# Kernel tuning notes

Hardware: AMD Instinct MI355X
Metric: run time of the kernel (lower is better)

The kernel has to match this reference:

```python
import jax, jax.numpy as jnp
import numpy as np

DIM = 768
HID = 3072  # 4 * DIM
EPS = 1e-5


def layer_norm(x, w, b):
    mu = jnp.mean(x, axis=-1, keepdims=True)
    var = jnp.var(x, axis=-1, keepdims=True)
    return (x - mu) * jax.lax.rsqrt(var + EPS) * w + b


def setup_inputs() -> dict:
    key = jax.random.key(0)
    ks = jax.random.split(key, 8)
    C, H = DIM, HID
    s = lambda fan_in: 1.0 / np.sqrt(fan_in)
    return {
        "x": jax.random.normal(ks[0], (32, 577, C), dtype=jnp.float32),
        "norm1_w": jnp.ones((C,), jnp.float32),
        "norm1_b": jnp.zeros((C,), jnp.float32),
        "qkv_w": jax.random.uniform(ks[1], (3 * C, C), jnp.float32, -s(C), s(C)),
        "proj_w": jax.random.uniform(ks[2], (C, C), jnp.float32, -s(C), s(C)),
        "proj_b": jax.random.uniform(ks[3], (C,), jnp.float32, -s(C), s(C)),
        "norm2_w": jnp.ones((C,), jnp.float32),
        "norm2_b": jnp.zeros((C,), jnp.float32),
        "fc1_w": jax.random.uniform(ks[4], (H, C), jnp.float32, -s(C), s(C)),
        "fc1_b": jax.random.uniform(ks[5], (H,), jnp.float32, -s(C), s(C)),
        "fc2_w": jax.random.uniform(ks[6], (C, H), jnp.float32, -s(H), s(H)),
        "fc2_b": jax.random.uniform(ks[7], (C,), jnp.float32, -s(H), s(H)),
    }


def reference(x, norm1_w, norm1_b, qkv_w, proj_w, proj_b,
              norm2_w, norm2_b, fc1_w, fc1_b, fc2_w, fc2_b):
    B, N, C = x.shape
    attn_size = int((N - 1) ** 0.5)
    scale = C ** -0.5

    # --- Attention on norm1(x) (single head) ---
    h = layer_norm(x, norm1_w, norm1_b)
    qkv = (h @ qkv_w.T).reshape(B, N, 3, C)           # [B,N,3,C]
    q, k, v = qkv[:, :, 0], qkv[:, :, 1], qkv[:, :, 2]
    attn = jax.nn.softmax(jnp.einsum('bnc,bmc->bnm', q, k) * scale, axis=-1)
    y = jnp.einsum('bnm,bmc->bnc', attn, v)           # [B,N,C]
    # Faithful to torch: .transpose(1,2).reshape(B,N,C) scrambles layout
    y = jnp.transpose(y, (0, 2, 1)).reshape(B, N, C)
    a = y @ proj_w.T + proj_b
    token_attn = attn[:, 0, 1:].reshape(B, 1, attn_size, attn_size)

    # Faithful to torch Block: input residual is discarded, attention out doubled
    x = a + a

    # --- MLP (exact GELU, as nn.GELU default) ---
    m = layer_norm(x, norm2_w, norm2_b)
    m = jax.nn.gelu(m @ fc1_w.T + fc1_b, approximate=False)
    m = m @ fc2_w.T + fc2_b
    x = x + m
    return (x, token_attn)
```

## Files before the change

### kernel.cpp

```cpp
#include <hip/hip_runtime.h>
#include <hip/hip_bf16.h>

#define Bz   32
#define Nn_  577
#define Np   640
#define Cc   768
#define Hh   3072
#define Mrows (Bz * Nn_)
#define OUT_X (Mrows * Cc)
#define SCALE 0.03608439182435161f

typedef unsigned short ushort_t;
typedef short short8 __attribute__((ext_vector_type(8)));
typedef float f32x4 __attribute__((ext_vector_type(4)));

__device__ __forceinline__ ushort_t f2b(float f) {
    __hip_bfloat16 h = __float2bfloat16(f);
    return *reinterpret_cast<ushort_t*>(&h);
}

__device__ __forceinline__ void gl16(const ushort_t* g, ushort_t* l) {
    __builtin_amdgcn_global_load_lds(
        (const __attribute__((address_space(1))) void*)g,
        (__attribute__((address_space(3))) void*)l, 16, 0, 0);
}

__device__ __forceinline__ float bsum(float v, float* sm) {
    #pragma unroll
    for (int o = 32; o > 0; o >>= 1) v += __shfl_down(v, o, 64);
    int lane = threadIdx.x & 63, wid = threadIdx.x >> 6;
    if (lane == 0) sm[wid] = v;
    __syncthreads();
    float r = sm[0] + sm[1] + sm[2] + sm[3];
    __syncthreads();
    return r;
}
__device__ __forceinline__ float bmax(float v, float* sm) {
    #pragma unroll
    for (int o = 32; o > 0; o >>= 1) v = fmaxf(v, __shfl_down(v, o, 64));
    int lane = threadIdx.x & 63, wid = threadIdx.x >> 6;
    if (lane == 0) sm[wid] = v;
    __syncthreads();
    float r = fmaxf(fmaxf(sm[0], sm[1]), fmaxf(sm[2], sm[3]));
    __syncthreads();
    return r;
}

__global__ void cvt_kernel(const float* __restrict__ in, ushort_t* __restrict__ out, int n) {
    int i = blockIdx.x * 256 + threadIdx.x;
    if (i < n) out[i] = f2b(in[i]);
}

__global__ void ln_bf16(const float* __restrict__ x, const float* __restrict__ w,
                        const float* __restrict__ b, ushort_t* __restrict__ out) {
    __shared__ float sm[8];
    long long row = blockIdx.x;
    const float* xr = x + row * Cc;
    float v[3]; float s = 0.f;
    #pragma unroll
    for (int i = 0; i < 3; ++i) { v[i] = xr[threadIdx.x + i * 256]; s += v[i]; }
    float mu = bsum(s, sm) * (1.f / (float)Cc);
    float sq = 0.f;
    #pragma unroll
    for (int i = 0; i < 3; ++i) { float d = v[i] - mu; sq += d * d; }
    float var = bsum(sq, sm + 4) * (1.f / (float)Cc);
    float inv = rsqrtf(var + 1e-5f);
    ushort_t* orow = out + row * Cc;
    #pragma unroll
    for (int i = 0; i < 3; ++i) {
        int c = threadIdx.x + i * 256;
        orow[c] = f2b((v[i] - mu) * inv * w[c] + b[c]);
    }
}

__global__ void softmax_bf16(const float* __restrict__ Sf, ushort_t* __restrict__ Sb,
                             float* __restrict__ tok) {
    __shared__ float sm[8];
    long long row = blockIdx.x;
    int b_l = (int)(row / Nn_), r = (int)(row - (long long)b_l * Nn_);
    const float* src = Sf + row * Np;
    ushort_t* dst = Sb + row * Np;
    float v[3]; float mx = -1e30f;
    #pragma unroll
    for (int i = 0; i < 3; ++i) {
        int c = threadIdx.x + i * 256;
        v[i] = (c < Nn_) ? src[c] : -1e30f;
        mx = fmaxf(mx, v[i]);
    }
    mx = bmax(mx, sm);
    float s = 0.f;
    #pragma unroll
    for (int i = 0; i < 3; ++i) {
        int c = threadIdx.x + i * 256;
        v[i] = (c < Nn_) ? expf(v[i] - mx) : 0.f;
        s += v[i];
    }
    s = bsum(s, sm + 4);
    float inv = 1.f / s;
    #pragma unroll
    for (int i = 0; i < 3; ++i) {
        int c = threadIdx.x + i * 256;
        float p = v[i] * inv;
        if (c < Np) dst[c] = (c < Nn_) ? f2b(p) : (ushort_t)0;
        if (r == 0 && c >= 1 && c < Nn_) tok[(long long)b_l * 576 + (c - 1)] = p;
    }
}

#define EPS_STORE 0
#define EPS_X2    1
#define EPS_GELU  2
#define EPS_ACC   3
#define EPS_QKV   4

template<int EPI, typename OutT>
__global__ __launch_bounds__(256)
void mm_bf16(const ushort_t* __restrict__ A, long long sAb, int lda, int M,
             const ushort_t* __restrict__ B, long long sBb, int ldb, int Nv,
             const float* __restrict__ bias,
             OutT* __restrict__ O, long long sOb, int ldo,
             int K, float alpha,
             ushort_t* __restrict__ qQ, ushort_t* __restrict__ qK, ushort_t* __restrict__ qV)
{
    __shared__ __align__(16) ushort_t As[128 * 32];
    __shared__ __align__(16) ushort_t Bs[128 * 32];
    const int z = blockIdx.z;
    A += (long long)z * sAb; B += (long long)z * sBb;
    if (O) O += (long long)z * sOb;
    const int n0 = blockIdx.x * 128;
    const int m0 = blockIdx.y * 128;
    const int tid = threadIdx.x;
    const int lane = tid & 63;
    const int wv = tid >> 6;
    const int wr = (wv >> 1) << 6;
    const int wc = (wv & 1) << 6;
    const int fr = lane & 15;
    const int koff = (lane >> 4) * 8;

    const int e0 = tid * 8, e1 = 2048 + tid * 8;
    const int ra0 = e0 >> 5, ca0 = e0 & 31;
    const int ra1 = e1 >> 5, ca1 = e1 & 31;
    const ushort_t* Ag0 = A + (long long)min(m0 + ra0, M - 1) * lda + ca0;
    const ushort_t* Ag1 = A + (long long)min(m0 + ra1, M - 1) * lda + ca1;
    const ushort_t* Bg0 = B + (long long)min(n0 + ra0, Nv - 1) * ldb + ca0;
    const ushort_t* Bg1 = B + (long long)min(n0 + ra1, Nv - 1) * ldb + ca1;

    f32x4 acc[4][4] = {};

    for (int k0 = 0; k0 < K; k0 += 32) {
        gl16(Ag0 + k0, &As[e0]);
        gl16(Ag1 + k0, &As[e1]);
        gl16(Bg0 + k0, &Bs[e0]);
        gl16(Bg1 + k0, &Bs[e1]);
        __syncthreads();
        short8 af[4], bfr[4];
        #pragma unroll
        for (int i = 0; i < 4; ++i)
            af[i] = *(const short8*)&As[(wr + i * 16 + fr) * 32 + koff];
        #pragma unroll
        for (int j = 0; j < 4; ++j)
            bfr[j] = *(const short8*)&Bs[(wc + j * 16 + fr) * 32 + koff];
        #pragma unroll
        for (int i = 0; i < 4; ++i)
            #pragma unroll
            for (int j = 0; j < 4; ++j)
                acc[i][j] = __builtin_amdgcn_mfma_f32_16x16x32_bf16(af[i], bfr[j], acc[i][j], 0, 0, 0);
        __syncthreads();
    }

    #pragma unroll
    for (int i = 0; i < 4; ++i) {
        int mb = m0 + wr + i * 16 + (lane >> 4) * 4;
        #pragma unroll
        for (int j = 0; j < 4; ++j) {
            int n = n0 + wc + j * 16 + fr;
            if (n >= Nv) continue;
            f32x4 v4 = acc[i][j];
            #pragma unroll
            for (int r = 0; r < 4; ++r) {
                int m = mb + r;
                if (m >= M) continue;
                float v = v4[r] * alpha;
                if constexpr (EPI == EPS_QKV) {
                    int b_l = m / Nn_, rr = m - b_l * Nn_;
                    if (n < Cc)            qQ[(long long)m * Cc + n] = f2b(v);
                    else if (n < 2 * Cc)   qK[(long long)m * Cc + (n - Cc)] = f2b(v);
                    else                   qV[((long long)b_l * Cc + (n - 2 * Cc)) * Np + rr] = f2b(v);
                } else {
                    if (bias) v += bias[n];
                    if constexpr (EPI == EPS_X2) v *= 2.f;
                    if constexpr (EPI == EPS_GELU) v = 0.5f * v * (1.f + erff(v * 0.70710678118654752f));
                    long long oi = (long long)m * ldo + n;
                    if constexpr (EPI == EPS_ACC) {
                        O[oi] += v;
                    } else {
                        if constexpr (sizeof(OutT) == 2) O[oi] = (OutT)f2b(v);
                        else                             O[oi] = (OutT)v;
                    }
                }
            }
        }
    }
}

extern "C" void kernel_launch(void* const* d_in, const int* in_sizes, int n_in,
                              void* d_out, int out_size, void* d_ws, size_t ws_size,
                              hipStream_t stream) {
    const float* x      = (const float*)d_in[0];
    const float* n1w    = (const float*)d_in[1];
    const float* n1b    = (const float*)d_in[2];
    const float* qkv_w  = (const float*)d_in[3];
    const float* proj_w = (const float*)d_in[4];
    const float* proj_b = (const float*)d_in[5];
    const float* n2w    = (const float*)d_in[6];
    const float* n2b    = (const float*)d_in[7];
    const float* fc1w   = (const float*)d_in[8];
    const float* fc1b   = (const float*)d_in[9];
    const float* fc2w   = (const float*)d_in[10];
    const float* fc2b   = (const float*)d_in[11];
    float* out = (float*)d_out;
    float* x2  = out;
    float* tok = out + OUT_X;

    char* ws = (char*)d_ws;
    const long long nWq = (long long)3 * Cc * Cc;
    const long long nWp = (long long)Cc * Cc;
    const long long nW1 = (long long)Hh * Cc;
    const long long nW2 = (long long)Cc * Hh;
    ushort_t* wq = (ushort_t*)ws;
    ushort_t* wp = wq + nWq;
    ushort_t* w1 = wp + nWp;
    ushort_t* w2 = w1 + nW1;
    const long long WBYTES = 2 * (nWq + nWp + nW1 + nW2);
    char* dyn = ws + WBYTES;
    long long avail = (long long)ws_size - WBYTES;

    const long long perG = 3LL * Nn_ * Cc * 2 + (long long)Cc * Np * 2
                         + (long long)Nn_ * Np * 4 + (long long)Nn_ * Np * 2;
    int G = 1;
    { const int o[5] = {16, 8, 4, 2, 1};
      for (int i = 0; i < 5; ++i) if ((long long)o[i] * perG <= avail) { G = o[i]; break; } }
    int CH = Nn_;
    { const int o[5] = {16, 8, 4, 2, 1};
      for (int i = 0; i < 5; ++i) if ((long long)o[i] * Nn_ * (Cc + Hh) * 2 <= avail) { CH = o[i] * Nn_; break; } }

    ushort_t* hbf = (ushort_t*)dyn;
    ushort_t* Q   = hbf + (long long)G * Nn_ * Cc;
    ushort_t* Kb  = Q   + (long long)G * Nn_ * Cc;
    ushort_t* Vt  = Kb  + (long long)G * Nn_ * Cc;
    float*    Sf  = (float*)(Vt + (long long)G * Cc * Np);
    ushort_t* Sb  = (ushort_t*)(Sf + (long long)G * Nn_ * Np);
    ushort_t* Yt  = hbf;
    ushort_t* g = (ushort_t*)dyn;
    ushort_t* t = g + (long long)CH * Cc;

    cvt_kernel<<<(int)((nWq + 255) / 256), 256, 0, stream>>>(qkv_w, wq, (int)nWq);
    cvt_kernel<<<(int)((nWp + 255) / 256), 256, 0, stream>>>(proj_w, wp, (int)nWp);
    cvt_kernel<<<(int)((nW1 + 255) / 256), 256, 0, stream>>>(fc1w, w1, (int)nW1);
    cvt_kernel<<<(int)((nW2 + 255) / 256), 256, 0, stream>>>(fc2w, w2, (int)nW2);

    for (int b0 = 0; b0 < Bz; b0 += G) {
        const int MR = G * Nn_;
        const int myM = (MR + 127) / 128;

        ln_bf16<<<MR, 256, 0, stream>>>(x + (long long)b0 * Nn_ * Cc, n1w, n1b, hbf);

        mm_bf16<EPS_QKV, float><<<dim3(18, myM, 1), 256, 0, stream>>>(
            hbf, 0, Cc, MR, wq, 0, Cc, 3 * Cc, nullptr,
            (float*)nullptr, 0, 0, Cc, 1.f, Q, Kb, Vt);

        mm_bf16<EPS_STORE, float><<<dim3(5, 5, G), 256, 0, stream>>>(
            Q, (long long)Nn_ * Cc, Cc, Nn_, Kb, (long long)Nn_ * Cc, Cc, Nn_, nullptr,
            Sf, (long long)Nn_ * Np, Np, Cc, SCALE, nullptr, nullptr, nullptr);

        softmax_bf16<<<MR, 256, 0, stream>>>(Sf, Sb, tok + (long long)b0 * 576);

        mm_bf16<EPS_STORE, ushort_t><<<dim3(5, 6, G), 256, 0, stream>>>(
            Vt, (long long)Cc * Np, Np, Cc, Sb, (long long)Nn_ * Np, Np, Nn_, nullptr,
            Yt, (long long)Cc * Nn_, Nn_, Np, 1.f, nullptr, nullptr, nullptr);

        mm_bf16<EPS_X2, float><<<dim3(6, myM, 1), 256, 0, stream>>>(
            Yt, 0, Cc, MR, wp, 0, Cc, Cc, proj_b,
            x2 + (long long)b0 * Nn_ * Cc, 0, Cc, Cc, 1.f, nullptr, nullptr, nullptr);
    }

    for (int c0 = 0; c0 < Mrows; c0 += CH) {
        const int myC = (CH + 127) / 128;

        ln_bf16<<<CH, 256, 0, stream>>>(x2 + (long long)c0 * Cc, n2w, n2b, g);

        mm_bf16<EPS_GELU, ushort_t><<<dim3(24, myC, 1), 256, 0, stream>>>(
            g, 0, Cc, CH, w1, 0, Cc, Hh, fc1b,
            t, 0, Hh, Cc, 1.f, nullptr, nullptr, nullptr);

        mm_bf16<EPS_ACC, float><<<dim3(6, myC, 1), 256, 0, stream>>>(
            t, 0, Hh, CH, w2, 0, Hh, Cc, fc2b,
            x2 + (long long)c0 * Cc, 0, Cc, Hh, 1.f, nullptr, nullptr, nullptr);
    }
}
```

Baseline: 1.010 ms.

## Swizzle LDS tiles, split-K fc2 with atomics, allow larger batch groups

XOR-swizzles the 8-element column chunks of the A/B shared-memory tiles by row so the MFMA fragment reads avoid LDS bank conflicts. Splits the fc2 GEMM into two K halves over blockIdx.z and accumulates into the residual with float atomicAdd, with bias added only by z==0. This doubles the block count for the small-N fc2 GEMM. It also lets the attention group size and MLP chunk size reach 32 batches and handles a partial final chunk. Atomics make the summation order nondeterministic and add contention on the output.

```diff
diff --git a/kernel.cpp b/kernel.cpp
--- a/kernel.cpp
+++ b/kernel.cpp
@@ -106,11 +106,11 @@
     }
 }
 
-#define EPS_STORE 0
-#define EPS_X2    1
-#define EPS_GELU  2
-#define EPS_ACC   3
-#define EPS_QKV   4
+#define EPS_STORE  0
+#define EPS_X2     1
+#define EPS_GELU   2
+#define EPS_ATOMIC 3
+#define EPS_QKV    4
 
 template<int EPI, typename OutT>
 __global__ __launch_bounds__(256)
@@ -134,15 +134,15 @@
     const int wr = (wv >> 1) << 6;
     const int wc = (wv & 1) << 6;
     const int fr = lane & 15;
-    const int koff = (lane >> 4) * 8;
+    const int kq = lane >> 4;
 
     const int e0 = tid * 8, e1 = 2048 + tid * 8;
-    const int ra0 = e0 >> 5, ca0 = e0 & 31;
-    const int ra1 = e1 >> 5, ca1 = e1 & 31;
-    const ushort_t* Ag0 = A + (long long)min(m0 + ra0, M - 1) * lda + ca0;
-    const ushort_t* Ag1 = A + (long long)min(m0 + ra1, M - 1) * lda + ca1;
-    const ushort_t* Bg0 = B + (long long)min(n0 + ra0, Nv - 1) * ldb + ca0;
-    const ushort_t* Bg1 = B + (long long)min(n0 + ra1, Nv - 1) * ldb + ca1;
+    const int ra0 = e0 >> 5, qa0 = (((e0 & 31) >> 3) ^ (ra0 & 3)) << 3;
+    const int ra1 = e1 >> 5, qa1 = (((e1 & 31) >> 3) ^ (ra1 & 3)) << 3;
+    const ushort_t* Ag0 = A + (long long)min(m0 + ra0, M - 1) * lda + qa0;
+    const ushort_t* Ag1 = A + (long long)min(m0 + ra1, M - 1) * lda + qa1;
+    const ushort_t* Bg0 = B + (long long)min(n0 + ra0, Nv - 1) * ldb + qa0;
+    const ushort_t* Bg1 = B + (long long)min(n0 + ra1, Nv - 1) * ldb + qa1;
 
     f32x4 acc[4][4] = {};
 
@@ -154,11 +154,15 @@
         __syncthreads();
         short8 af[4], bfr[4];
         #pragma unroll
-        for (int i = 0; i < 4; ++i)
-            af[i] = *(const short8*)&As[(wr + i * 16 + fr) * 32 + koff];
+        for (int i = 0; i < 4; ++i) {
+            int r = wr + i * 16 + fr;
+            af[i] = *(const short8*)&As[r * 32 + ((kq ^ (r & 3)) << 3)];
+        }
         #pragma unroll
-        for (int j = 0; j < 4; ++j)
-            bfr[j] = *(const short8*)&Bs[(wc + j * 16 + fr) * 32 + koff];
+        for (int j = 0; j < 4; ++j) {
+            int r = wc + j * 16 + fr;
+            bfr[j] = *(const short8*)&Bs[r * 32 + ((kq ^ (r & 3)) << 3)];
+        }
         #pragma unroll
         for (int i = 0; i < 4; ++i)
             #pragma unroll
@@ -185,17 +189,16 @@
                     if (n < Cc)            qQ[(long long)m * Cc + n] = f2b(v);
                     else if (n < 2 * Cc)   qK[(long long)m * Cc + (n - Cc)] = f2b(v);
                     else                   qV[((long long)b_l * Cc + (n - 2 * Cc)) * Np + rr] = f2b(v);
+                } else if constexpr (EPI == EPS_ATOMIC) {
+                    if (bias && z == 0) v += bias[n];
+                    atomicAdd(&O[(long long)m * ldo + n], v);
                 } else {
                     if (bias) v += bias[n];
                     if constexpr (EPI == EPS_X2) v *= 2.f;
                     if constexpr (EPI == EPS_GELU) v = 0.5f * v * (1.f + erff(v * 0.70710678118654752f));
                     long long oi = (long long)m * ldo + n;
-                    if constexpr (EPI == EPS_ACC) {
-                        O[oi] += v;
-                    } else {
-                        if constexpr (sizeof(OutT) == 2) O[oi] = (OutT)f2b(v);
-                        else                             O[oi] = (OutT)v;
-                    }
+                    if constexpr (sizeof(OutT) == 2) O[oi] = (OutT)f2b(v);
+                    else                             O[oi] = (OutT)v;
                 }
             }
         }
@@ -237,11 +240,11 @@
     const long long perG = 3LL * Nn_ * Cc * 2 + (long long)Cc * Np * 2
                          + (long long)Nn_ * Np * 4 + (long long)Nn_ * Np * 2;
     int G = 1;
-    { const int o[5] = {16, 8, 4, 2, 1};
-      for (int i = 0; i < 5; ++i) if ((long long)o[i] * perG <= avail) { G = o[i]; break; } }
+    { const int o[6] = {32, 16, 8, 4, 2, 1};
+      for (int i = 0; i < 6; ++i) if ((long long)o[i] * perG <= avail) { G = o[i]; break; } }
     int CH = Nn_;
-    { const int o[5] = {16, 8, 4, 2, 1};
-      for (int i = 0; i < 5; ++i) if ((long long)o[i] * Nn_ * (Cc + Hh) * 2 <= avail) { CH = o[i] * Nn_; break; } }
+    { const int o[6] = {32, 16, 8, 4, 2, 1};
+      for (int i = 0; i < 6; ++i) if ((long long)o[i] * Nn_ * (Cc + Hh) * 2 <= avail) { CH = o[i] * Nn_; break; } }
 
     ushort_t* hbf = (ushort_t*)dyn;
     ushort_t* Q   = hbf + (long long)G * Nn_ * Cc;
@@ -284,16 +287,17 @@
     }
 
     for (int c0 = 0; c0 < Mrows; c0 += CH) {
-        const int myC = (CH + 127) / 128;
-
-        ln_bf16<<<CH, 256, 0, stream>>>(x2 + (long long)c0 * Cc, n2w, n2b, g);
+        const int cn = (Mrows - c0 < CH) ? (Mrows - c0) : CH;
+        const int myC = (cn + 127) / 128;
+
+        ln_bf16<<<cn, 256, 0, stream>>>(x2 + (long long)c0 * Cc, n2w, n2b, g);
 
         mm_bf16<EPS_GELU, ushort_t><<<dim3(24, myC, 1), 256, 0, stream>>>(
-            g, 0, Cc, CH, w1, 0, Cc, Hh, fc1b,
+            g, 0, Cc, cn, w1, 0, Cc, Hh, fc1b,
             t, 0, Hh, Cc, 1.f, nullptr, nullptr, nullptr);
 
-        mm_bf16<EPS_ACC, float><<<dim3(6, myC, 1), 256, 0, stream>>>(
-            t, 0, Hh, CH, w2, 0, Hh, Cc, fc2b,
-            x2 + (long long)c0 * Cc, 0, Cc, Hh, 1.f, nullptr, nullptr, nullptr);
-    }
-}
+        mm_bf16<EPS_ATOMIC, float><<<dim3(6, myC, 2), 256, 0, stream>>>(
+            t, Hh / 2, Hh, cn, w2, Hh / 2, Hh, Cc, fc2b,
+            x2 + (long long)c0 * Cc, 0, Cc, Hh / 2, 1.f, nullptr, nullptr, nullptr);
+    }
+}
```

Result: faster. 921.8 us (-8.7%).
